# Kernel tuning notes

Measured on AMD Instinct MI355X. Metric: run time of the kernel, lower is better.

The kernel has to match this reference:

```python
import jax, jax.numpy as jnp
import numpy as np

H = 256   # hidden size
U = 10    # attention units


def _lstm_cell(xt, h, c, Wih, Whh, bih, bhh):
    # PyTorch gate order: i, f, g, o
    gates = xt @ Wih.T + h @ Whh.T + bih + bhh          # [B, 4H]
    i, f, g, o = jnp.split(gates, 4, axis=-1)
    i = jax.nn.sigmoid(i); f = jax.nn.sigmoid(f)
    g = jnp.tanh(g);       o = jax.nn.sigmoid(o)
    c = f * c + i * g
    h = o * jnp.tanh(c)
    return h, c


def setup_inputs() -> dict:
    key = jax.random.key(0)
    ks = jax.random.split(key, 12)
    B, S = 512, 256
    s = 1.0 / np.sqrt(H)
    x = jax.random.normal(ks[0], (B, S), dtype=jnp.float32)
    y = jax.random.randint(ks[1], (B, S), 0, S, dtype=jnp.int64)
    return {
        "x": x,
        "y": y,
        "enc_Wih": jax.random.uniform(ks[2], (4 * H, 1), jnp.float32, -s, s),
        "enc_Whh": jax.random.uniform(ks[3], (4 * H, H), jnp.float32, -s, s),
        "enc_bih": jax.random.uniform(ks[4], (4 * H,), jnp.float32, -s, s),
        "enc_bhh": jax.random.uniform(ks[5], (4 * H,), jnp.float32, -s, s),
        "dec_Wih": jax.random.uniform(ks[6], (4 * H, H + 1), jnp.float32, -s, s),
        "dec_Whh": jax.random.uniform(ks[7], (4 * H, H), jnp.float32, -s, s),
        "dec_bih": jax.random.uniform(ks[8], (4 * H,), jnp.float32, -s, s),
        "dec_bhh": jax.random.uniform(ks[9], (4 * H,), jnp.float32, -s, s),
        "att_W1": jax.random.uniform(ks[10], (U, H), jnp.float32, -s, s),
        "att_W2": jax.random.uniform(ks[11], (U, H), jnp.float32, -s, s),
        "att_V": jax.random.uniform(jax.random.fold_in(key, 99), (1, U), jnp.float32, -s, s),
    }


def reference(x, y, enc_Wih, enc_Whh, enc_bih, enc_bhh,
              dec_Wih, dec_Whh, dec_bih, dec_bhh,
              att_W1, att_W2, att_V):
    B, S = x.shape

    # ---- Encoder: LSTM over sequence of scalar inputs ----
    def enc_step(carry, xt):  # xt: [B, 1]
        h, c = carry
        h, c = _lstm_cell(xt, h, c, enc_Wih, enc_Whh, enc_bih, enc_bhh)
        return (h, c), h

    h0 = jnp.zeros((B, H), x.dtype)
    (hN, cN), enc_out_t = jax.lax.scan(enc_step, (h0, h0), x.T[:, :, None])
    enc_out = jnp.transpose(enc_out_t, (1, 0, 2))            # [B, S, H]

    # precompute W1 @ encoder_hidden (same math, hoisted out of loop)
    encW1 = jnp.einsum('bsh,uh->bsu', enc_out, att_W1)       # [B, S, U]

    # ---- Decoder loop (teacher forcing with ratio 1.0) ----
    def dec_step(carry, y_t):
        h, c, dec_in = carry                                  # dec_in: [B, 1]
        u = jnp.tanh(encW1 + (h @ att_W2.T)[:, None, :])      # [B, S, U]
        logits = jnp.einsum('bsu,ou->bso', u, att_V)[..., 0]  # [B, S]
        aj = jax.nn.softmax(logits, axis=1)
        di = jnp.einsum('bs,bsh->bh', aj, enc_out)            # [B, H]
        lstm_in = jnp.concatenate([di, dec_in], axis=1)       # [B, H+1]
        h, c = _lstm_cell(lstm_in, h, c, dec_Wih, dec_Whh, dec_bih, dec_bhh)
        pred = jnp.argmax(logits, axis=1)                     # [B]
        logp = jax.nn.log_softmax(logits, axis=1)
        loss_t = -jnp.mean(jnp.take_along_axis(logp, y_t[:, None], axis=1))
        dec_in_next = jnp.take_along_axis(x, y_t[:, None], axis=1)  # teacher force
        return (h, c, dec_in_next), (pred, loss_t)

    dec_in0 = jnp.zeros((B, 1), x.dtype)
    _, (preds, losses) = jax.lax.scan(dec_step, (hN, cN, dec_in0), y.T)
    outputs = preds[:, :, None].astype(jnp.int64)             # [S, B, 1]
    batch_loss = jnp.sum(losses) / B
    return outputs, batch_loss
```

## Files before the change

kernel.cpp:

```cpp
#include <hip/hip_runtime.h>
#include <cmath>

__device__ __forceinline__ double dexp_(double x) {
    x = fmin(fmax(x, -64.0), 64.0);
    double w = x * 1.4426950408889634;
    double n = rint(w);
    double u = (w - n) * 0.6931471805599453;
    double p = 1.0 + u * (1.0 + u * (0.5 + u * (1.6666666666666666e-01 +
               u * (4.1666666666666664e-02 + u * (8.3333333333333332e-03 +
               u * (1.3888888888888889e-03 + u * (1.9841269841269841e-04 +
               u * (2.4801587301587302e-05 + u * (2.7557319223985893e-06 +
               u * (2.7557319223985888e-07 + u * 2.5052108385441720e-08))))))))));
    return ldexp(p, (int)n);
}
__device__ __forceinline__ double dtanh_(double x) {
    double ax = fabs(x);
    double e = dexp_(2.0 * ax);
    double t = 1.0 - 2.0 / (e + 1.0);
    return copysign(t, x);
}
__device__ __forceinline__ double dsig_(double x) {
    return 1.0 / (1.0 + dexp_(-x));
}

__global__ __launch_bounds__(256) void prep_kernel(
    const float* __restrict__ eWih, const float* __restrict__ eWhh,
    const float* __restrict__ ebih, const float* __restrict__ ebhh,
    const float* __restrict__ dWih, const float* __restrict__ dWhh,
    const float* __restrict__ dbih, const float* __restrict__ dbhh,
    float* __restrict__ WencR, double* __restrict__ bencR,
    float* __restrict__ WdecR, double* __restrict__ bdecR)
{
    const int n_enc = 257 * 1024;
    const int n_dec = 513 * 1024;
    const int total = n_enc + n_dec + 2048;
    for (int idx = blockIdx.x * blockDim.x + threadIdx.x; idx < total;
         idx += gridDim.x * blockDim.x) {
        if (idx < n_enc) {
            int k = idx >> 10, c = idx & 1023;
            int j = c >> 2, g = c & 3, r = g * 256 + j;
            WencR[idx] = (k == 0) ? eWih[r] : eWhh[r * 256 + (k - 1)];
        } else if (idx < n_enc + n_dec) {
            int i2 = idx - n_enc;
            int k = i2 >> 10, c = i2 & 1023;
            int j = c >> 2, g = c & 3, r = g * 256 + j;
            WdecR[i2] = (k < 257) ? dWih[r * 257 + k] : dWhh[r * 256 + (k - 257)];
        } else {
            int c = idx - n_enc - n_dec;
            if (c < 1024) {
                int r = (c & 3) * 256 + (c >> 2);
                bencR[c] = (double)ebih[r] + (double)ebhh[r];
            } else {
                int c2 = c - 1024;
                int r = (c2 & 3) * 256 + (c2 >> 2);
                bdecR[c2] = (double)dbih[r] + (double)dbhh[r];
            }
        }
    }
}

__global__ __launch_bounds__(256) void lstm_enc_kernel(
    const float* __restrict__ x, const float* __restrict__ W,
    const double* __restrict__ bR, const float* __restrict__ h_in, long hin_str,
    float* __restrict__ h_out,
    float* __restrict__ c_st, int t)
{
    __shared__ float Xs[16 * 260];
    const int tid = threadIdx.x;
    const int row = tid & 15;
    const int jt  = tid >> 4;
    const int b0  = (blockIdx.x & 31) * 16;
    const int jg  = (blockIdx.x >> 5) * 16 + jt;

    #pragma unroll
    for (int i = 0; i < 4; ++i) {
        int idx = tid + i * 256;
        int r = idx >> 6;
        int c4 = (idx & 63) * 4;
        float4 v = *(const float4*)&h_in[(long)(b0 + r) * hin_str + c4];
        *(float4*)&Xs[r * 260 + c4] = v;
    }
    if (tid < 16) Xs[tid * 260 + 256] = x[(b0 + tid) * 256 + t];
    __syncthreads();

    const float* wp = W + jg * 4;
    double A0 = 0, A1 = 0, A2 = 0, A3 = 0;
    const float* xr = &Xs[row * 260];
    for (int k0 = 0; k0 < 256; k0 += 8) {
        float4 w[8];
        #pragma unroll
        for (int i = 0; i < 8; ++i)
            w[i] = *(const float4*)&wp[(1 + k0 + i) * 1024];
        float4 xa = *(const float4*)&xr[k0];
        float4 xb = *(const float4*)&xr[k0 + 4];
        float xs[8] = {xa.x, xa.y, xa.z, xa.w, xb.x, xb.y, xb.z, xb.w};
        float s0 = 0.f, s1 = 0.f, s2 = 0.f, s3 = 0.f;
        #pragma unroll
        for (int i = 0; i < 8; ++i) {
            s0 = fmaf(w[i].x, xs[i], s0);
            s1 = fmaf(w[i].y, xs[i], s1);
            s2 = fmaf(w[i].z, xs[i], s2);
            s3 = fmaf(w[i].w, xs[i], s3);
        }
        A0 += (double)s0; A1 += (double)s1;
        A2 += (double)s2; A3 += (double)s3;
    }
    {
        float4 w = *(const float4*)&wp[0];
        float xv = xr[256];
        A0 += (double)(w.x * xv); A1 += (double)(w.y * xv);
        A2 += (double)(w.z * xv); A3 += (double)(w.w * xv);
    }

    double bi = bR[jg * 4 + 0], bf = bR[jg * 4 + 1];
    double bg = bR[jg * 4 + 2], bo = bR[jg * 4 + 3];
    int b = b0 + row;
    double iv = dsig_(A0 + bi);
    double fv = dsig_(A1 + bf);
    double gv = dtanh_(A2 + bg);
    double ov = dsig_(A3 + bo);
    long ci = (long)b * 256 + jg;
    double c = fv * (double)c_st[ci] + iv * gv;
    c_st[ci] = (float)c;
    h_out[(long)b * 65536 + jg] = (float)(ov * dtanh_(c));
}

__global__ __launch_bounds__(256) void encW1_kernel(
    const float* __restrict__ enc_out, const float* __restrict__ W1,
    double* __restrict__ encW1d)
{
    __shared__ float sa[64][260];
    __shared__ float sw[10][257];
    const int tid = threadIdx.x;
    const int m0 = blockIdx.x * 64;
    #pragma unroll
    for (int i = 0; i < 16; ++i) {
        int idx = tid + i * 256;
        int row = idx >> 6;
        int c4 = (idx & 63) * 4;
        const float4 v = *(const float4*)&enc_out[(long)(m0 + row) * 256 + c4];
        *(float4*)&sa[row][c4] = v;
    }
    for (int i = tid; i < 2560; i += 256) sw[i >> 8][i & 255] = W1[i];
    __syncthreads();
    for (int o = tid; o < 640; o += 256) {
        int r = o / 10;
        int u = o - r * 10;
        double acc = 0.0;
        #pragma unroll 4
        for (int k = 0; k < 256; ++k)
            acc += (double)sa[r][k] * (double)sw[u][k];
        encW1d[(long)(m0 + r) * 10 + u] = acc;
    }
}

__global__ __launch_bounds__(256) void att_kernel(
    const double* __restrict__ encW1d, const float* __restrict__ enc_out,
    const float* __restrict__ W2, const float* __restrict__ V,
    const float* __restrict__ h_in, long hin_str, const int* __restrict__ y,
    float* __restrict__ di, float* __restrict__ logp_buf,
    float* __restrict__ out_pred, int t)
{
    const int b = blockIdx.x;
    const int s = threadIdx.x;
    const int wid = s >> 6, lane = s & 63;

    __shared__ float s_h[256];
    __shared__ double s_V[12];
    __shared__ double s_W2h[12];
    __shared__ double s_ld[256];
    __shared__ float s_e[256];
    __shared__ double s_red[4];
    __shared__ int s_redi[4];
    __shared__ double s_maxd, s_Zd;
    __shared__ int s_am;

    s_h[s] = h_in[(long)b * hin_str + s];
    if (s < 10) s_V[s] = (double)V[s];
    __syncthreads();

    for (int u = wid; u < 10; u += 4) {
        double p = 0.0;
        #pragma unroll
        for (int i = 0; i < 4; ++i) {
            int k = lane + i * 64;
            p += (double)W2[u * 256 + k] * (double)s_h[k];
        }
        #pragma unroll
        for (int off = 32; off >= 1; off >>= 1) p += __shfl_down(p, off, 64);
        if (lane == 0) s_W2h[u] = p;
    }
    __syncthreads();

    const double* eW = encW1d + ((long)b * 256 + s) * 10;
    double l = 0.0;
    #pragma unroll
    for (int u = 0; u < 10; ++u) l += s_V[u] * dtanh_(eW[u] + s_W2h[u]);
    s_ld[s] = l;

    {
        double v = l; int idx = s;
        #pragma unroll
        for (int off = 32; off >= 1; off >>= 1) {
            double v2 = __shfl_down(v, off, 64);
            int i2 = __shfl_down(idx, off, 64);
            if (v2 > v || (v2 == v && i2 < idx)) { v = v2; idx = i2; }
        }
        if (lane == 0) { s_red[wid] = v; s_redi[wid] = idx; }
    }
    __syncthreads();
    if (s == 0) {
        double v = s_red[0]; int idx = s_redi[0];
        #pragma unroll
        for (int w = 1; w < 4; ++w) {
            if (s_red[w] > v || (s_red[w] == v && s_redi[w] < idx)) {
                v = s_red[w]; idx = s_redi[w];
            }
        }
        s_maxd = v; s_am = idx;
    }
    __syncthreads();

    double e = dexp_(l - s_maxd);
    s_e[s] = (float)e;
    {
        double v = e;
        #pragma unroll
        for (int off = 32; off >= 1; off >>= 1) v += __shfl_down(v, off, 64);
        if (lane == 0) s_red[wid] = v;
    }
    __syncthreads();
    if (s == 0) {
        double Z = s_red[0] + s_red[1] + s_red[2] + s_red[3];
        s_Zd = Z;
        out_pred[t * 512 + b] = (float)s_am;
        int yv = y[b * 256 + t];
        logp_buf[t * 512 + b] = (float)(s_ld[yv] - s_maxd - log(Z));
    }
    __syncthreads();

    const float rcpZ = (float)(1.0 / s_Zd);
    const float* ep = enc_out + (long)b * 65536 + s;
    float acc0 = 0.f, acc1 = 0.f, acc2 = 0.f, acc3 = 0.f;
    for (int s2 = 0; s2 < 256; s2 += 4) {
        acc0 += s_e[s2 + 0] * ep[(s2 + 0) * 256];
        acc1 += s_e[s2 + 1] * ep[(s2 + 1) * 256];
        acc2 += s_e[s2 + 2] * ep[(s2 + 2) * 256];
        acc3 += s_e[s2 + 3] * ep[(s2 + 3) * 256];
    }
    di[b * 256 + s] = ((acc0 + acc1) + (acc2 + acc3)) * rcpZ;
}

__global__ __launch_bounds__(256) void lstm_dec_kernel(
    const float* __restrict__ x, const int* __restrict__ y,
    const float* __restrict__ W, const double* __restrict__ bR,
    const float* __restrict__ di, const float* __restrict__ h_in, long hin_str,
    float* __restrict__ h_out, float* __restrict__ c_st, int t)
{
    __shared__ float Xs[16 * 516];
    const int tid = threadIdx.x;
    const int row = tid & 15;
    const int jt  = tid >> 4;
    const int b0  = (blockIdx.x & 31) * 16;
    const int jg  = (blockIdx.x >> 5) * 16 + jt;

    #pragma unroll
    for (int i = 0; i < 4; ++i) {
        int idx = tid + i * 256;
        int r = idx >> 6;
        int c4 = (idx & 63) * 4;
        float4 v = *(const float4*)&di[(long)(b0 + r) * 256 + c4];
        *(float4*)&Xs[r * 516 + c4] = v;
        float4 u = *(const float4*)&h_in[(long)(b0 + r) * hin_str + c4];
        *(float4*)&Xs[r * 516 + 260 + c4] = u;
    }
    if (tid < 16) {
        int b = b0 + tid;
        float dv = 0.0f;
        if (t > 0) {
            int yi = y[b * 256 + (t - 1)];
            dv = x[b * 256 + yi];
        }
        Xs[tid * 516 + 256] = dv;
    }
    __syncthreads();

    const float* wp = W + jg * 4;
    double A0 = 0, A1 = 0, A2 = 0, A3 = 0;
    const float* xr = &Xs[row * 516];

    for (int k0 = 0; k0 < 256; k0 += 8) {
        float4 w[8];
        #pragma unroll
        for (int i = 0; i < 8; ++i)
            w[i] = *(const float4*)&wp[(k0 + i) * 1024];
        float4 xa = *(const float4*)&xr[k0];
        float4 xb = *(const float4*)&xr[k0 + 4];
        float xs[8] = {xa.x, xa.y, xa.z, xa.w, xb.x, xb.y, xb.z, xb.w};
        float s0 = 0.f, s1 = 0.f, s2 = 0.f, s3 = 0.f;
        #pragma unroll
        for (int i = 0; i < 8; ++i) {
            s0 = fmaf(w[i].x, xs[i], s0);
            s1 = fmaf(w[i].y, xs[i], s1);
            s2 = fmaf(w[i].z, xs[i], s2);
            s3 = fmaf(w[i].w, xs[i], s3);
        }
        A0 += (double)s0; A1 += (double)s1;
        A2 += (double)s2; A3 += (double)s3;
    }
    {
        float4 w = *(const float4*)&wp[256 * 1024];
        float xv = xr[256];
        A0 += (double)(w.x * xv); A1 += (double)(w.y * xv);
        A2 += (double)(w.z * xv); A3 += (double)(w.w * xv);
    }
    for (int k0 = 0; k0 < 256; k0 += 8) {
        float4 w[8];
        #pragma unroll
        for (int i = 0; i < 8; ++i)
            w[i] = *(const float4*)&wp[(257 + k0 + i) * 1024];
        float4 xa = *(const float4*)&xr[260 + k0];
        float4 xb = *(const float4*)&xr[260 + k0 + 4];
        float xs[8] = {xa.x, xa.y, xa.z, xa.w, xb.x, xb.y, xb.z, xb.w};
        float s0 = 0.f, s1 = 0.f, s2 = 0.f, s3 = 0.f;
        #pragma unroll
        for (int i = 0; i < 8; ++i) {
            s0 = fmaf(w[i].x, xs[i], s0);
            s1 = fmaf(w[i].y, xs[i], s1);
            s2 = fmaf(w[i].z, xs[i], s2);
            s3 = fmaf(w[i].w, xs[i], s3);
        }
        A0 += (double)s0; A1 += (double)s1;
        A2 += (double)s2; A3 += (double)s3;
    }

    double bi = bR[jg * 4 + 0], bf = bR[jg * 4 + 1];
    double bg = bR[jg * 4 + 2], bo = bR[jg * 4 + 3];
    int b = b0 + row;
    double iv = dsig_(A0 + bi);
    double fv = dsig_(A1 + bf);
    double gv = dtanh_(A2 + bg);
    double ov = dsig_(A3 + bo);
    long ci = (long)b * 256 + jg;
    double c = fv * (double)c_st[ci] + iv * gv;
    c_st[ci] = (float)c;
    h_out[ci] = (float)(ov * dtanh_(c));
}

__global__ __launch_bounds__(256) void loss_kernel(
    const float* __restrict__ logp_buf, float* __restrict__ out)
{
    const int tid = threadIdx.x;
    double acc = 0.0;
    for (int i = tid; i < 131072; i += 256) acc += (double)logp_buf[i];
    __shared__ double s_red[4];
    const int wid = tid >> 6, lane = tid & 63;
    #pragma unroll
    for (int off = 32; off >= 1; off >>= 1) acc += __shfl_down(acc, off, 64);
    if (lane == 0) s_red[wid] = acc;
    __syncthreads();
    if (tid == 0) {
        out[131072] = (float)(-(s_red[0] + s_red[1] + s_red[2] + s_red[3])
                              / (512.0 * 512.0));
    }
}

extern "C" void kernel_launch(void* const* d_in, const int* in_sizes, int n_in,
                              void* d_out, int out_size, void* d_ws, size_t ws_size,
                              hipStream_t stream)
{
    const float* x    = (const float*)d_in[0];
    const int*   y    = (const int*)  d_in[1];
    const float* eWih = (const float*)d_in[2];
    const float* eWhh = (const float*)d_in[3];
    const float* ebih = (const float*)d_in[4];
    const float* ebhh = (const float*)d_in[5];
    const float* dWih = (const float*)d_in[6];
    const float* dWhh = (const float*)d_in[7];
    const float* dbih = (const float*)d_in[8];
    const float* dbhh = (const float*)d_in[9];
    const float* W1   = (const float*)d_in[10];
    const float* W2   = (const float*)d_in[11];
    const float* V    = (const float*)d_in[12];

    double* encW1d = (double*)d_ws;
    double* bencR  = encW1d + 1310720;
    double* bdecR  = bencR + 1024;
    float* enc_out = (float*)(bdecR + 1024);
    float* c_st    = enc_out + 33554432;
    float* hzero   = c_st + 131072;
    float* hd      = hzero + 131072;
    float* dibuf   = hd + 262144;
    float* logp    = dibuf + 131072;
    float* WencR   = logp + 131072;
    float* WdecR   = WencR + 263168;

    float* out = (float*)d_out;

    hipMemsetAsync(c_st, 0, 131072 * sizeof(float), stream);
    hipMemsetAsync(hzero, 0, 131072 * sizeof(float), stream);

    prep_kernel<<<512, 256, 0, stream>>>(eWih, eWhh, ebih, ebhh,
                                         dWih, dWhh, dbih, dbhh,
                                         WencR, bencR, WdecR, bdecR);

    for (int t = 0; t < 256; ++t) {
        const float* hin; long hstr;
        if (t == 0) { hin = hzero; hstr = 256; }
        else        { hin = enc_out + (long)(t - 1) * 256; hstr = 65536; }
        lstm_enc_kernel<<<512, 256, 0, stream>>>(x, WencR, bencR, hin, hstr,
                                                 enc_out + (long)t * 256, c_st, t);
    }

    encW1_kernel<<<2048, 256, 0, stream>>>(enc_out, W1, encW1d);

    for (int t = 0; t < 256; ++t) {
        const float* hin; long hstr;
        if (t == 0) { hin = enc_out + 255 * 256; hstr = 65536; }
        else        { hin = hd + (t & 1) * 131072; hstr = 256; }
        float* hout = hd + ((t + 1) & 1) * 131072;
        att_kernel<<<512, 256, 0, stream>>>(encW1d, enc_out, W2, V, hin, hstr,
                                            y, dibuf, logp, out, t);
        lstm_dec_kernel<<<512, 256, 0, stream>>>(x, y, WdecR, bdecR, dibuf,
                                                 hin, hstr, hout, c_st, t);
    }

    loss_kernel<<<1, 256, 0, stream>>>(logp, out);
}
```

Baseline: 19.85 ms.

## Fuse encoder and decoder time loops into persistent per-batch-group kernels

Replaces the 256 encoder launches and 512 decoder launches with one persistent kernel each. Every block owns 4 batch rows for all timesteps and keeps h and c in LDS and registers. This removes per-step launch overhead and global round-trips of the hidden state. In exchange only 128 blocks run, each thread streams the full weight column every step, and attention runs serially over the 4 batch rows with many block barriers, so parallelism and occupancy drop sharply.

```diff
diff --git a/kernel.cpp b/kernel.cpp
--- a/kernel.cpp
+++ b/kernel.cpp
@@ -59,70 +59,86 @@
     }
 }
 
-__global__ __launch_bounds__(256) void lstm_enc_kernel(
+__global__ __launch_bounds__(256) void enc_fused_kernel(
     const float* __restrict__ x, const float* __restrict__ W,
-    const double* __restrict__ bR, const float* __restrict__ h_in, long hin_str,
-    float* __restrict__ h_out,
-    float* __restrict__ c_st, int t)
-{
-    __shared__ float Xs[16 * 260];
+    const double* __restrict__ bR, float* __restrict__ enc_out,
+    float* __restrict__ c_st)
+{
+    __shared__ float h_lds[2][4][256];
+    __shared__ float xs[2][4];
     const int tid = threadIdx.x;
-    const int row = tid & 15;
-    const int jt  = tid >> 4;
-    const int b0  = (blockIdx.x & 31) * 16;
-    const int jg  = (blockIdx.x >> 5) * 16 + jt;
-
-    #pragma unroll
-    for (int i = 0; i < 4; ++i) {
-        int idx = tid + i * 256;
-        int r = idx >> 6;
-        int c4 = (idx & 63) * 4;
-        float4 v = *(const float4*)&h_in[(long)(b0 + r) * hin_str + c4];
-        *(float4*)&Xs[r * 260 + c4] = v;
-    }
-    if (tid < 16) Xs[tid * 260 + 256] = x[(b0 + tid) * 256 + t];
-    __syncthreads();
-
-    const float* wp = W + jg * 4;
-    double A0 = 0, A1 = 0, A2 = 0, A3 = 0;
-    const float* xr = &Xs[row * 260];
-    for (int k0 = 0; k0 < 256; k0 += 8) {
-        float4 w[8];
+    const int b0g = blockIdx.x * 4;
+
+    #pragma unroll
+    for (int bb = 0; bb < 4; ++bb) h_lds[0][bb][tid] = 0.0f;
+
+    float c_f[4] = {0.f, 0.f, 0.f, 0.f};
+    const double bi = bR[tid * 4 + 0], bf = bR[tid * 4 + 1];
+    const double bg = bR[tid * 4 + 2], bo = bR[tid * 4 + 3];
+    const float* wcol = W + tid * 4;
+
+    for (int t = 0; t < 256; ++t) {
+        const int cur = t & 1, nxt = cur ^ 1;
+        if (tid < 4) xs[cur][tid] = x[(b0g + tid) * 256 + t];
+        __syncthreads();
+
+        double A[4][4];
         #pragma unroll
-        for (int i = 0; i < 8; ++i)
-            w[i] = *(const float4*)&wp[(1 + k0 + i) * 1024];
-        float4 xa = *(const float4*)&xr[k0];
-        float4 xb = *(const float4*)&xr[k0 + 4];
-        float xs[8] = {xa.x, xa.y, xa.z, xa.w, xb.x, xb.y, xb.z, xb.w};
-        float s0 = 0.f, s1 = 0.f, s2 = 0.f, s3 = 0.f;
+        for (int bb = 0; bb < 4; ++bb) {
+            #pragma unroll
+            for (int g = 0; g < 4; ++g) A[bb][g] = 0.0;
+        }
+
+        for (int k0 = 0; k0 < 256; k0 += 8) {
+            float4 w[8];
+            #pragma unroll
+            for (int i = 0; i < 8; ++i)
+                w[i] = *(const float4*)&wcol[(1 + k0 + i) * 1024];
+            #pragma unroll
+            for (int bb = 0; bb < 4; ++bb) {
+                float4 xa = *(const float4*)&h_lds[cur][bb][k0];
+                float4 xb = *(const float4*)&h_lds[cur][bb][k0 + 4];
+                float xv[8] = {xa.x, xa.y, xa.z, xa.w, xb.x, xb.y, xb.z, xb.w};
+                float s0 = 0.f, s1 = 0.f, s2 = 0.f, s3 = 0.f;
+                #pragma unroll
+                for (int i = 0; i < 8; ++i) {
+                    s0 = fmaf(w[i].x, xv[i], s0);
+                    s1 = fmaf(w[i].y, xv[i], s1);
+                    s2 = fmaf(w[i].z, xv[i], s2);
+                    s3 = fmaf(w[i].w, xv[i], s3);
+                }
+                A[bb][0] += (double)s0; A[bb][1] += (double)s1;
+                A[bb][2] += (double)s2; A[bb][3] += (double)s3;
+            }
+        }
+        {
+            float4 w = *(const float4*)&wcol[0];
+            #pragma unroll
+            for (int bb = 0; bb < 4; ++bb) {
+                float xv = xs[cur][bb];
+                A[bb][0] += (double)(w.x * xv); A[bb][1] += (double)(w.y * xv);
+                A[bb][2] += (double)(w.z * xv); A[bb][3] += (double)(w.w * xv);
+            }
+        }
+
         #pragma unroll
-        for (int i = 0; i < 8; ++i) {
-            s0 = fmaf(w[i].x, xs[i], s0);
-            s1 = fmaf(w[i].y, xs[i], s1);
-            s2 = fmaf(w[i].z, xs[i], s2);
-            s3 = fmaf(w[i].w, xs[i], s3);
-        }
-        A0 += (double)s0; A1 += (double)s1;
-        A2 += (double)s2; A3 += (double)s3;
-    }
-    {
-        float4 w = *(const float4*)&wp[0];
-        float xv = xr[256];
-        A0 += (double)(w.x * xv); A1 += (double)(w.y * xv);
-        A2 += (double)(w.z * xv); A3 += (double)(w.w * xv);
-    }
-
-    double bi = bR[jg * 4 + 0], bf = bR[jg * 4 + 1];
-    double bg = bR[jg * 4 + 2], bo = bR[jg * 4 + 3];
-    int b = b0 + row;
-    double iv = dsig_(A0 + bi);
-    double fv = dsig_(A1 + bf);
-    double gv = dtanh_(A2 + bg);
-    double ov = dsig_(A3 + bo);
-    long ci = (long)b * 256 + jg;
-    double c = fv * (double)c_st[ci] + iv * gv;
-    c_st[ci] = (float)c;
-    h_out[(long)b * 65536 + jg] = (float)(ov * dtanh_(c));
+        for (int bb = 0; bb < 4; ++bb) {
+            double iv = dsig_(A[bb][0] + bi);
+            double fv = dsig_(A[bb][1] + bf);
+            double gv = dtanh_(A[bb][2] + bg);
+            double ov = dsig_(A[bb][3] + bo);
+            double c = fv * (double)c_f[bb] + iv * gv;
+            c_f[bb] = (float)c;
+            float hv = (float)(ov * dtanh_(c));
+            enc_out[(long)(b0g + bb) * 65536 + t * 256 + tid] = hv;
+            h_lds[nxt][bb][tid] = hv;
+        }
+        __syncthreads();
+    }
+
+    #pragma unroll
+    for (int bb = 0; bb < 4; ++bb)
+        c_st[(long)(b0g + bb) * 256 + tid] = c_f[bb];
 }
 
 __global__ __launch_bounds__(256) void encW1_kernel(
@@ -154,197 +170,215 @@
     }
 }
 
-__global__ __launch_bounds__(256) void att_kernel(
+__global__ __launch_bounds__(256) void dec_fused_kernel(
     const double* __restrict__ encW1d, const float* __restrict__ enc_out,
     const float* __restrict__ W2, const float* __restrict__ V,
-    const float* __restrict__ h_in, long hin_str, const int* __restrict__ y,
-    float* __restrict__ di, float* __restrict__ logp_buf,
-    float* __restrict__ out_pred, int t)
-{
-    const int b = blockIdx.x;
-    const int s = threadIdx.x;
-    const int wid = s >> 6, lane = s & 63;
-
-    __shared__ float s_h[256];
+    const float* __restrict__ x, const int* __restrict__ y,
+    const float* __restrict__ W, const double* __restrict__ bR,
+    const float* __restrict__ c_init, float* __restrict__ logp_buf,
+    float* __restrict__ out_pred)
+{
+    __shared__ float h_lds[2][4][256];
+    __shared__ float di_lds[4][256];
+    __shared__ float e_lds[4][256];
+    __shared__ float rcpZ_lds[4];
+    __shared__ float din_lds[4];
     __shared__ double s_V[12];
     __shared__ double s_W2h[12];
     __shared__ double s_ld[256];
-    __shared__ float s_e[256];
     __shared__ double s_red[4];
     __shared__ int s_redi[4];
-    __shared__ double s_maxd, s_Zd;
+    __shared__ double s_maxd;
     __shared__ int s_am;
 
-    s_h[s] = h_in[(long)b * hin_str + s];
-    if (s < 10) s_V[s] = (double)V[s];
+    const int tid = threadIdx.x;
+    const int wid = tid >> 6, lane = tid & 63;
+    const int b0g = blockIdx.x * 4;
+
+    if (tid < 10) s_V[tid] = (double)V[tid];
+    #pragma unroll
+    for (int bb = 0; bb < 4; ++bb)
+        h_lds[0][bb][tid] = enc_out[(long)(b0g + bb) * 65536 + 255 * 256 + tid];
+    float c_f[4];
+    #pragma unroll
+    for (int bb = 0; bb < 4; ++bb)
+        c_f[bb] = c_init[(long)(b0g + bb) * 256 + tid];
+    const double bi = bR[tid * 4 + 0], bf = bR[tid * 4 + 1];
+    const double bg = bR[tid * 4 + 2], bo = bR[tid * 4 + 3];
+    const float* wcol = W + tid * 4;
     __syncthreads();
 
-    for (int u = wid; u < 10; u += 4) {
-        double p = 0.0;
+    for (int t = 0; t < 256; ++t) {
+        const int cur = t & 1, nxt = cur ^ 1;
+
+        for (int bb = 0; bb < 4; ++bb) {
+            const int b = b0g + bb;
+            const float* hh = h_lds[cur][bb];
+
+            for (int u = wid; u < 10; u += 4) {
+                double p = 0.0;
+                #pragma unroll
+                for (int i = 0; i < 4; ++i) {
+                    int k = lane + i * 64;
+                    p += (double)W2[u * 256 + k] * (double)hh[k];
+                }
+                #pragma unroll
+                for (int off = 32; off >= 1; off >>= 1) p += __shfl_down(p, off, 64);
+                if (lane == 0) s_W2h[u] = p;
+            }
+            __syncthreads();
+
+            const double* eW = encW1d + ((long)b * 256 + tid) * 10;
+            double l = 0.0;
+            #pragma unroll
+            for (int u = 0; u < 10; ++u) l += s_V[u] * dtanh_(eW[u] + s_W2h[u]);
+            s_ld[tid] = l;
+
+            {
+                double v = l; int idx = tid;
+                #pragma unroll
+                for (int off = 32; off >= 1; off >>= 1) {
+                    double v2 = __shfl_down(v, off, 64);
+                    int i2 = __shfl_down(idx, off, 64);
+                    if (v2 > v || (v2 == v && i2 < idx)) { v = v2; idx = i2; }
+                }
+                if (lane == 0) { s_red[wid] = v; s_redi[wid] = idx; }
+            }
+            __syncthreads();
+            if (tid == 0) {
+                double v = s_red[0]; int idx = s_redi[0];
+                #pragma unroll
+                for (int w2 = 1; w2 < 4; ++w2) {
+                    if (s_red[w2] > v || (s_red[w2] == v && s_redi[w2] < idx)) {
+                        v = s_red[w2]; idx = s_redi[w2];
+                    }
+                }
+                s_maxd = v; s_am = idx;
+            }
+            __syncthreads();
+
+            double e = dexp_(l - s_maxd);
+            e_lds[bb][tid] = (float)e;
+            {
+                double v = e;
+                #pragma unroll
+                for (int off = 32; off >= 1; off >>= 1) v += __shfl_down(v, off, 64);
+                if (lane == 0) s_red[wid] = v;
+            }
+            __syncthreads();
+            if (tid == 0) {
+                double Z = s_red[0] + s_red[1] + s_red[2] + s_red[3];
+                rcpZ_lds[bb] = (float)(1.0 / Z);
+                out_pred[t * 512 + b] = (float)s_am;
+                int yv = y[b * 256 + t];
+                logp_buf[t * 512 + b] = (float)(s_ld[yv] - s_maxd - log(Z));
+            }
+            __syncthreads();
+        }
+
+        {
+            float acc[4][4];
+            #pragma unroll
+            for (int bb = 0; bb < 4; ++bb) {
+                #pragma unroll
+                for (int g = 0; g < 4; ++g) acc[bb][g] = 0.f;
+            }
+            for (int s2 = 0; s2 < 256; s2 += 4) {
+                #pragma unroll
+                for (int bb = 0; bb < 4; ++bb) {
+                    const float* ep = enc_out + (long)(b0g + bb) * 65536 + tid;
+                    acc[bb][0] += e_lds[bb][s2 + 0] * ep[(s2 + 0) * 256];
+                    acc[bb][1] += e_lds[bb][s2 + 1] * ep[(s2 + 1) * 256];
+                    acc[bb][2] += e_lds[bb][s2 + 2] * ep[(s2 + 2) * 256];
+                    acc[bb][3] += e_lds[bb][s2 + 3] * ep[(s2 + 3) * 256];
+                }
+            }
+            #pragma unroll
+            for (int bb = 0; bb < 4; ++bb)
+                di_lds[bb][tid] = ((acc[bb][0] + acc[bb][1]) +
+                                   (acc[bb][2] + acc[bb][3])) * rcpZ_lds[bb];
+        }
+        if (tid < 4) {
+            int b = b0g + tid;
+            float dv = 0.0f;
+            if (t > 0) { int yi = y[b * 256 + (t - 1)]; dv = x[b * 256 + yi]; }
+            din_lds[tid] = dv;
+        }
+        __syncthreads();
+
+        double A[4][4];
         #pragma unroll
-        for (int i = 0; i < 4; ++i) {
-            int k = lane + i * 64;
-            p += (double)W2[u * 256 + k] * (double)s_h[k];
-        }
+        for (int bb = 0; bb < 4; ++bb) {
+            #pragma unroll
+            for (int g = 0; g < 4; ++g) A[bb][g] = 0.0;
+        }
+
+        for (int k0 = 0; k0 < 256; k0 += 8) {
+            float4 w[8];
+            #pragma unroll
+            for (int i = 0; i < 8; ++i)
+                w[i] = *(const float4*)&wcol[(k0 + i) * 1024];
+            #pragma unroll
+            for (int bb = 0; bb < 4; ++bb) {
+                float4 xa = *(const float4*)&di_lds[bb][k0];
+                float4 xb = *(const float4*)&di_lds[bb][k0 + 4];
+                float xv[8] = {xa.x, xa.y, xa.z, xa.w, xb.x, xb.y, xb.z, xb.w};
+                float s0 = 0.f, s1 = 0.f, s2 = 0.f, s3 = 0.f;
+                #pragma unroll
+                for (int i = 0; i < 8; ++i) {
+                    s0 = fmaf(w[i].x, xv[i], s0);
+                    s1 = fmaf(w[i].y, xv[i], s1);
+                    s2 = fmaf(w[i].z, xv[i], s2);
+                    s3 = fmaf(w[i].w, xv[i], s3);
+                }
+                A[bb][0] += (double)s0; A[bb][1] += (double)s1;
+                A[bb][2] += (double)s2; A[bb][3] += (double)s3;
+            }
+        }
+        {
+            float4 w = *(const float4*)&wcol[256 * 1024];
+            #pragma unroll
+            for (int bb = 0; bb < 4; ++bb) {
+                float xv = din_lds[bb];
+                A[bb][0] += (double)(w.x * xv); A[bb][1] += (double)(w.y * xv);
+                A[bb][2] += (double)(w.z * xv); A[bb][3] += (double)(w.w * xv);
+            }
+        }
+        for (int k0 = 0; k0 < 256; k0 += 8) {
+            float4 w[8];
+            #pragma unroll
+            for (int i = 0; i < 8; ++i)
+                w[i] = *(const float4*)&wcol[(257 + k0 + i) * 1024];
+            #pragma unroll
+            for (int bb = 0; bb < 4; ++bb) {
+                float4 xa = *(const float4*)&h_lds[cur][bb][k0];
+                float4 xb = *(const float4*)&h_lds[cur][bb][k0 + 4];
+                float xv[8] = {xa.x, xa.y, xa.z, xa.w, xb.x, xb.y, xb.z, xb.w};
+                float s0 = 0.f, s1 = 0.f, s2 = 0.f, s3 = 0.f;
+                #pragma unroll
+                for (int i = 0; i < 8; ++i) {
+                    s0 = fmaf(w[i].x, xv[i], s0);
+                    s1 = fmaf(w[i].y, xv[i], s1);
+                    s2 = fmaf(w[i].z, xv[i], s2);
+                    s3 = fmaf(w[i].w, xv[i], s3);
+                }
+                A[bb][0] += (double)s0; A[bb][1] += (double)s1;
+                A[bb][2] += (double)s2; A[bb][3] += (double)s3;
+            }
+        }
+
         #pragma unroll
-        for (int off = 32; off >= 1; off >>= 1) p += __shfl_down(p, off, 64);
-        if (lane == 0) s_W2h[u] = p;
-    }
-    __syncthreads();
-
-    const double* eW = encW1d + ((long)b * 256 + s) * 10;
-    double l = 0.0;
-    #pragma unroll
-    for (int u = 0; u < 10; ++u) l += s_V[u] * dtanh_(eW[u] + s_W2h[u]);
-    s_ld[s] = l;
-
-    {
-        double v = l; int idx = s;
-        #pragma unroll
-        for (int off = 32; off >= 1; off >>= 1) {
-            double v2 = __shfl_down(v, off, 64);
-            int i2 = __shfl_down(idx, off, 64);
-            if (v2 > v || (v2 == v && i2 < idx)) { v = v2; idx = i2; }
-        }
-        if (lane == 0) { s_red[wid] = v; s_redi[wid] = idx; }
-    }
-    __syncthreads();
-    if (s == 0) {
-        double v = s_red[0]; int idx = s_redi[0];
-        #pragma unroll
-        for (int w = 1; w < 4; ++w) {
-            if (s_red[w] > v || (s_red[w] == v && s_redi[w] < idx)) {
-                v = s_red[w]; idx = s_redi[w];
-            }
-        }
-        s_maxd = v; s_am = idx;
-    }
-    __syncthreads();
-
-    double e = dexp_(l - s_maxd);
-    s_e[s] = (float)e;
-    {
-        double v = e;
-        #pragma unroll
-        for (int off = 32; off >= 1; off >>= 1) v += __shfl_down(v, off, 64);
-        if (lane == 0) s_red[wid] = v;
-    }
-    __syncthreads();
-    if (s == 0) {
-        double Z = s_red[0] + s_red[1] + s_red[2] + s_red[3];
-        s_Zd = Z;
-        out_pred[t * 512 + b] = (float)s_am;
-        int yv = y[b * 256 + t];
-        logp_buf[t * 512 + b] = (float)(s_ld[yv] - s_maxd - log(Z));
-    }
-    __syncthreads();
-
-    const float rcpZ = (float)(1.0 / s_Zd);
-    const float* ep = enc_out + (long)b * 65536 + s;
-    float acc0 = 0.f, acc1 = 0.f, acc2 = 0.f, acc3 = 0.f;
-    for (int s2 = 0; s2 < 256; s2 += 4) {
-        acc0 += s_e[s2 + 0] * ep[(s2 + 0) * 256];
-        acc1 += s_e[s2 + 1] * ep[(s2 + 1) * 256];
-        acc2 += s_e[s2 + 2] * ep[(s2 + 2) * 256];
-        acc3 += s_e[s2 + 3] * ep[(s2 + 3) * 256];
-    }
-    di[b * 256 + s] = ((acc0 + acc1) + (acc2 + acc3)) * rcpZ;
-}
-
-__global__ __launch_bounds__(256) void lstm_dec_kernel(
-    const float* __restrict__ x, const int* __restrict__ y,
-    const float* __restrict__ W, const double* __restrict__ bR,
-    const float* __restrict__ di, const float* __restrict__ h_in, long hin_str,
-    float* __restrict__ h_out, float* __restrict__ c_st, int t)
-{
-    __shared__ float Xs[16 * 516];
-    const int tid = threadIdx.x;
-    const int row = tid & 15;
-    const int jt  = tid >> 4;
-    const int b0  = (blockIdx.x & 31) * 16;
-    const int jg  = (blockIdx.x >> 5) * 16 + jt;
-
-    #pragma unroll
-    for (int i = 0; i < 4; ++i) {
-        int idx = tid + i * 256;
-        int r = idx >> 6;
-        int c4 = (idx & 63) * 4;
-        float4 v = *(const float4*)&di[(long)(b0 + r) * 256 + c4];
-        *(float4*)&Xs[r * 516 + c4] = v;
-        float4 u = *(const float4*)&h_in[(long)(b0 + r) * hin_str + c4];
-        *(float4*)&Xs[r * 516 + 260 + c4] = u;
-    }
-    if (tid < 16) {
-        int b = b0 + tid;
-        float dv = 0.0f;
-        if (t > 0) {
-            int yi = y[b * 256 + (t - 1)];
-            dv = x[b * 256 + yi];
-        }
-        Xs[tid * 516 + 256] = dv;
-    }
-    __syncthreads();
-
-    const float* wp = W + jg * 4;
-    double A0 = 0, A1 = 0, A2 = 0, A3 = 0;
-    const float* xr = &Xs[row * 516];
-
-    for (int k0 = 0; k0 < 256; k0 += 8) {
-        float4 w[8];
-        #pragma unroll
-        for (int i = 0; i < 8; ++i)
-            w[i] = *(const float4*)&wp[(k0 + i) * 1024];
-        float4 xa = *(const float4*)&xr[k0];
-        float4 xb = *(const float4*)&xr[k0 + 4];
-        float xs[8] = {xa.x, xa.y, xa.z, xa.w, xb.x, xb.y, xb.z, xb.w};
-        float s0 = 0.f, s1 = 0.f, s2 = 0.f, s3 = 0.f;
-        #pragma unroll
-        for (int i = 0; i < 8; ++i) {
-            s0 = fmaf(w[i].x, xs[i], s0);
-            s1 = fmaf(w[i].y, xs[i], s1);
-            s2 = fmaf(w[i].z, xs[i], s2);
-            s3 = fmaf(w[i].w, xs[i], s3);
-        }
-        A0 += (double)s0; A1 += (double)s1;
-        A2 += (double)s2; A3 += (double)s3;
-    }
-    {
-        float4 w = *(const float4*)&wp[256 * 1024];
-        float xv = xr[256];
-        A0 += (double)(w.x * xv); A1 += (double)(w.y * xv);
-        A2 += (double)(w.z * xv); A3 += (double)(w.w * xv);
-    }
-    for (int k0 = 0; k0 < 256; k0 += 8) {
-        float4 w[8];
-        #pragma unroll
-        for (int i = 0; i < 8; ++i)
-            w[i] = *(const float4*)&wp[(257 + k0 + i) * 1024];
-        float4 xa = *(const float4*)&xr[260 + k0];
-        float4 xb = *(const float4*)&xr[260 + k0 + 4];
-        float xs[8] = {xa.x, xa.y, xa.z, xa.w, xb.x, xb.y, xb.z, xb.w};
-        float s0 = 0.f, s1 = 0.f, s2 = 0.f, s3 = 0.f;
-        #pragma unroll
-        for (int i = 0; i < 8; ++i) {
-            s0 = fmaf(w[i].x, xs[i], s0);
-            s1 = fmaf(w[i].y, xs[i], s1);
-            s2 = fmaf(w[i].z, xs[i], s2);
-            s3 = fmaf(w[i].w, xs[i], s3);
-        }
-        A0 += (double)s0; A1 += (double)s1;
-        A2 += (double)s2; A3 += (double)s3;
-    }
-
-    double bi = bR[jg * 4 + 0], bf = bR[jg * 4 + 1];
-    double bg = bR[jg * 4 + 2], bo = bR[jg * 4 + 3];
-    int b = b0 + row;
-    double iv = dsig_(A0 + bi);
-    double fv = dsig_(A1 + bf);
-    double gv = dtanh_(A2 + bg);
-    double ov = dsig_(A3 + bo);
-    long ci = (long)b * 256 + jg;
-    double c = fv * (double)c_st[ci] + iv * gv;
-    c_st[ci] = (float)c;
-    h_out[ci] = (float)(ov * dtanh_(c));
+        for (int bb = 0; bb < 4; ++bb) {
+            double iv = dsig_(A[bb][0] + bi);
+            double fv = dsig_(A[bb][1] + bf);
+            double gv = dtanh_(A[bb][2] + bg);
+            double ov = dsig_(A[bb][3] + bo);
+            double c = fv * (double)c_f[bb] + iv * gv;
+            c_f[bb] = (float)c;
+            h_lds[nxt][bb][tid] = (float)(ov * dtanh_(c));
+        }
+        __syncthreads();
+    }
 }
 
 __global__ __launch_bounds__(256) void loss_kernel(
@@ -397,33 +431,16 @@
 
     float* out = (float*)d_out;
 
-    hipMemsetAsync(c_st, 0, 131072 * sizeof(float), stream);
-    hipMemsetAsync(hzero, 0, 131072 * sizeof(float), stream);
-
     prep_kernel<<<512, 256, 0, stream>>>(eWih, eWhh, ebih, ebhh,
                                          dWih, dWhh, dbih, dbhh,
                                          WencR, bencR, WdecR, bdecR);
 
-    for (int t = 0; t < 256; ++t) {
-        const float* hin; long hstr;
-        if (t == 0) { hin = hzero; hstr = 256; }
-        else        { hin = enc_out + (long)(t - 1) * 256; hstr = 65536; }
-        lstm_enc_kernel<<<512, 256, 0, stream>>>(x, WencR, bencR, hin, hstr,
-                                                 enc_out + (long)t * 256, c_st, t);
-    }
+    enc_fused_kernel<<<128, 256, 0, stream>>>(x, WencR, bencR, enc_out, c_st);
 
     encW1_kernel<<<2048, 256, 0, stream>>>(enc_out, W1, encW1d);
 
-    for (int t = 0; t < 256; ++t) {
-        const float* hin; long hstr;
-        if (t == 0) { hin = enc_out + 255 * 256; hstr = 65536; }
-        else        { hin = hd + (t & 1) * 131072; hstr = 256; }
-        float* hout = hd + ((t + 1) & 1) * 131072;
-        att_kernel<<<512, 256, 0, stream>>>(encW1d, enc_out, W2, V, hin, hstr,
-                                            y, dibuf, logp, out, t);
-        lstm_dec_kernel<<<512, 256, 0, stream>>>(x, y, WdecR, bdecR, dibuf,
-                                                 hin, hstr, hout, c_st, t);
-    }
+    dec_fused_kernel<<<128, 256, 0, stream>>>(encW1d, enc_out, W2, V, x, y,
+                                              WdecR, bdecR, c_st, logp, out);
 
     loss_kernel<<<1, 256, 0, stream>>>(logp, out);
 }
```

After: 24.00 ms. 1.21x slower.
